# Kernel optimization log

Hardware: AMD Instinct MI355X
Metric: run time of the kernel (lower is better)

## Reference

```python
import jax, jax.numpy as jnp
import numpy as np

B, T, C = 2, 2048, 2048
N_HEAD, N_KV_HEAD = 16, 4
HEAD_DIM = C // N_HEAD  # 128
N_REP = N_HEAD // N_KV_HEAD  # 4


def setup_inputs() -> dict:
    key = jax.random.key(0)
    ks = jax.random.split(key, 5)
    x = jax.random.normal(ks[0], (B, T, C), dtype=jnp.float32)
    # RoPE freqs (theta=10000), real cos/sin form of torch's complex freqs_cis
    inv_freq = 1.0 / (10000.0 ** (jnp.arange(0, HEAD_DIM, 2, dtype=jnp.float32) / HEAD_DIM))
    angles = jnp.arange(T, dtype=jnp.float32)[:, None] * inv_freq[None, :]  # [T, HEAD_DIM//2]
    freqs_cos = jnp.cos(angles)
    freqs_sin = jnp.sin(angles)
    s = 0.02
    wq = jax.random.normal(ks[1], (C, C), dtype=jnp.float32) * s
    wk = jax.random.normal(ks[2], (N_KV_HEAD * HEAD_DIM, C), dtype=jnp.float32) * s
    wv = jax.random.normal(ks[3], (N_KV_HEAD * HEAD_DIM, C), dtype=jnp.float32) * s
    wo = jax.random.normal(ks[4], (C, C), dtype=jnp.float32) * s
    return {"x": x, "freqs_cos": freqs_cos, "freqs_sin": freqs_sin,
            "wq": wq, "wk": wk, "wv": wv, "wo": wo}


def _apply_rotary(t, cos, sin):
    # t: [B, T, H, D]; pairs (even, odd) treated as complex, multiplied by cos+i*sin
    tr = t.reshape(*t.shape[:-1], -1, 2)  # [B,T,H,D/2,2]
    t0, t1 = tr[..., 0], tr[..., 1]
    c = cos[None, :, None, :]  # [1,T,1,D/2]
    s = sin[None, :, None, :]
    out = jnp.stack([t0 * c - t1 * s, t0 * s + t1 * c], axis=-1)
    return out.reshape(t.shape)


def reference(x, freqs_cos, freqs_sin, wq, wk, wv, wo):
    b, t, _ = x.shape
    xq = (x @ wq.T).reshape(b, t, N_HEAD, HEAD_DIM)
    xk = (x @ wk.T).reshape(b, t, N_KV_HEAD, HEAD_DIM)
    xv = (x @ wv.T).reshape(b, t, N_KV_HEAD, HEAD_DIM)
    xq = _apply_rotary(xq, freqs_cos, freqs_sin)
    xk = _apply_rotary(xk, freqs_cos, freqs_sin)
    # GQA: repeat_interleave kv heads to n_head
    xk_r = jnp.repeat(xk, N_REP, axis=2)
    xv_r = jnp.repeat(xv, N_REP, axis=2)
    # [B,H,T,D]
    q = xq.transpose(0, 2, 1, 3)
    k = xk_r.transpose(0, 2, 1, 3)
    v = xv_r.transpose(0, 2, 1, 3)
    scale = 1.0 / jnp.sqrt(jnp.float32(HEAD_DIM))
    scores = jnp.einsum('bhtd,bhsd->bhts', q, k) * scale
    causal = jnp.tril(jnp.ones((t, t), dtype=bool))
    scores = jnp.where(causal[None, None], scores, jnp.finfo(scores.dtype).min)
    attn = jax.nn.softmax(scores, axis=-1)
    y = jnp.einsum('bhts,bhsd->bhtd', attn, v)
    y = y.transpose(0, 2, 1, 3).reshape(b, t, C)
    return y @ wo.T
```

## Files before the change

kernel.cpp:

```cpp
#include <hip/hip_runtime.h>

typedef __attribute__((ext_vector_type(8))) __bf16 bf16x8;
typedef __attribute__((ext_vector_type(4))) __bf16 bf16x4;
typedef __attribute__((ext_vector_type(4))) float floatx4;

#define MFMA16x16x32 __builtin_amdgcn_mfma_f32_16x16x32_bf16

__device__ __forceinline__ void async_load16(const void* g, void* l) {
  __builtin_amdgcn_global_load_lds((const __attribute__((address_space(1))) void*)g,
                                   (__attribute__((address_space(3))) void*)l, 16, 0, 0);
}

__global__ __launch_bounds__(256) void cast_all_kernel(const float* __restrict__ x,
                                                       const float* __restrict__ wq,
                                                       const float* __restrict__ wk,
                                                       const float* __restrict__ wv,
                                                       const float* __restrict__ wo,
                                                       __bf16* __restrict__ dst) {
  int i = blockIdx.x * blockDim.x + threadIdx.x;
  const float* src;
  int off;
  if (i < 2097152)      { src = x;  off = 0; }
  else if (i < 3145728) { src = wq; off = 2097152; }
  else if (i < 3407872) { src = wk; off = 3145728; }
  else if (i < 3670016) { src = wv; off = 3407872; }
  else                  { src = wo; off = 3670016; }
  float4 v = ((const float4*)src)[i - off];
  bf16x4 o;
  o[0] = (__bf16)v.x; o[1] = (__bf16)v.y; o[2] = (__bf16)v.z; o[3] = (__bf16)v.w;
  *(bf16x4*)(dst + (size_t)i * 4) = o;
}

template <int MODE, int BN>
__global__ __launch_bounds__(512, 1) void gemm_bt(const __bf16* __restrict__ A,
                                                  const __bf16* __restrict__ Bw,
                                                  float* __restrict__ C,
                                                  const float* __restrict__ cs,
                                                  const float* __restrict__ sn,
                                                  __bf16* __restrict__ qb,
                                                  __bf16* __restrict__ kb,
                                                  __bf16* __restrict__ vtg,
                                                  int M, int N, int K) {
  constexpr int NW = BN / 4;
  constexpr int NF = NW / 16;
  constexpr int NBI = BN / 64;
  __shared__ __bf16 As[2][256][64];
  __shared__ __bf16 Bs[2][BN][64];
  const int tid = threadIdx.x;
  const int wave = tid >> 6, lane = tid & 63;
  const int quad = lane >> 4, l16 = lane & 15;
  const int wm2 = wave >> 2, wn4 = wave & 3;
  const int lr = lane >> 3, ls = lane & 7;
  const int segg = ls ^ lr;

  const int nwg = gridDim.x;
  const int wg = (blockIdx.x & 7) * (nwg >> 3) + (blockIdx.x >> 3);
  const int GY = M >> 8;
  const int by = wg % GY, bx = wg / GY;
  const int row0 = by * 256, col0 = bx * BN;

  floatx4 acc[8][NF] = {};
  const __bf16* Ab = A + (size_t)row0 * K + segg * 8;
  const __bf16* Bb = Bw + (size_t)col0 * K + segg * 8;

  auto stage = [&](int sb, int k0) {
#pragma unroll
    for (int i = 0; i < 4; i++)
      async_load16(Ab + (size_t)(wave * 32 + i * 8 + lr) * K + k0,
                   &As[sb][wave * 32 + i * 8][0]);
#pragma unroll
    for (int j = 0; j < NBI; j++)
      async_load16(Bb + (size_t)(wave * (BN / 8) + j * 8 + lr) * K + k0,
                   &Bs[sb][wave * (BN / 8) + j * 8][0]);
  };

  const int NS = K >> 6;
  stage(0, 0);
  stage(1, 64);

#pragma unroll 2
  for (int s = 0; s < NS; s++) {
    const int c = s & 1;
    if (s == NS - 1) {
      asm volatile("s_waitcnt vmcnt(0)" ::: "memory");
    } else if constexpr (NBI == 3) {
      asm volatile("s_waitcnt vmcnt(7)" ::: "memory");
    } else {
      asm volatile("s_waitcnt vmcnt(6)" ::: "memory");
    }
    __builtin_amdgcn_s_barrier();

    bf16x8 af[2][8], bfr[2][NF];
#pragma unroll
    for (int kk = 0; kk < 2; kk++) {
#pragma unroll
      for (int mt = 0; mt < 8; mt++) {
        int row = wm2 * 128 + mt * 16 + l16;
        int seg = (kk * 4 + quad) ^ (row & 7);
        af[kk][mt] = *(const bf16x8*)&As[c][row][seg * 8];
      }
#pragma unroll
      for (int nt = 0; nt < NF; nt++) {
        int row = wn4 * NW + nt * 16 + l16;
        int seg = (kk * 4 + quad) ^ (row & 7);
        bfr[kk][nt] = *(const bf16x8*)&Bs[c][row][seg * 8];
      }
    }
    asm volatile("s_waitcnt lgkmcnt(0)" ::: "memory");
    __builtin_amdgcn_s_barrier();
    if (s + 2 < NS) stage(c, (s + 2) * 64);
    __builtin_amdgcn_s_setprio(1);
#pragma unroll
    for (int kk = 0; kk < 2; kk++)
#pragma unroll
      for (int mt = 0; mt < 8; mt++)
#pragma unroll
        for (int nt = 0; nt < NF; nt++)
          acc[mt][nt] = MFMA16x16x32(af[kk][mt], bfr[kk][nt], acc[mt][nt], 0, 0, 0);
    __builtin_amdgcn_s_setprio(0);
  }

  if (MODE == 0) {
#pragma unroll
    for (int mt = 0; mt < 8; mt++)
#pragma unroll
      for (int nt = 0; nt < NF; nt++)
#pragma unroll
        for (int r = 0; r < 4; r++) {
          int row = row0 + wm2 * 128 + mt * 16 + quad * 4 + r;
          int col = col0 + wn4 * NW + nt * 16 + l16;
          C[(size_t)row * N + col] = acc[mt][nt][r];
        }
  } else {
#pragma unroll
    for (int mt = 0; mt < 8; mt++)
#pragma unroll
      for (int nt = 0; nt < NF; nt++) {
        const int cbase = col0 + wn4 * NW + nt * 16;
        if (cbase < 2560) {
          const int c = cbase + l16;
#pragma unroll
          for (int r = 0; r < 4; r++) {
            int row = row0 + wm2 * 128 + mt * 16 + quad * 4 + r;
            int t = row & 2047;
            float v = acc[mt][nt][r];
            float vp = __shfl_xor(v, 1);
            int i = (c & 127) >> 1;
            float co = cs[t * 64 + i], si = sn[t * 64 + i];
            float rv = v * co + ((c & 1) ? vp : -vp) * si;
            if (cbase < 2048) {
              qb[(size_t)row * 2048 + c] = (__bf16)(rv * 0.1275411391f);
            } else {
              kb[(size_t)row * 512 + c - 2048] = (__bf16)rv;
            }
          }
        }
      }
    __bf16* Vl = &As[0][0][0] + wave * 2048;
    const int brow = row0 + wm2 * 128;
    const int bb = brow >> 11, trow = brow & 2047;
#pragma unroll
    for (int nt = 0; nt < NF; nt++) {
      const int cbase = col0 + wn4 * NW + nt * 16;
      if (cbase >= 2560) {
#pragma unroll
        for (int mt = 0; mt < 8; mt++)
#pragma unroll
          for (int r = 0; r < 4; r++)
            Vl[l16 * 128 + mt * 16 + quad * 4 + r] = (__bf16)acc[mt][nt][r];
        asm volatile("" ::: "memory");
        const int vB = cbase - 2560;
#pragma unroll
        for (int p = 0; p < 4; p++) {
          int vd = p * 4 + (lane >> 4);
          int t0 = (lane & 15) * 8;
          bf16x8 val = *(const bf16x8*)&Vl[vd * 128 + t0];
          *(bf16x8*)&vtg[((size_t)bb * 512 + vB + vd) * 2048 + trow + t0] = val;
        }
        asm volatile("" ::: "memory");
      }
    }
  }
}

__global__ __launch_bounds__(256, 2) void attn_kernel(const __bf16* __restrict__ qb,
                                                      const __bf16* __restrict__ kb,
                                                      const __bf16* __restrict__ vtg,
                                                      __bf16* __restrict__ yb) {
  const int id = blockIdx.x;
  const int kvh = id & 3, b = (id >> 2) & 1;
  const int pair = (id >> 3) & 1;
  const int tile = 63 - (id >> 4);
  const int tid = threadIdx.x, wave = tid >> 6, lane = tid & 63;
  const int ck = wave >> 1, hw = wave & 1;
  const int h = kvh * 4 + pair * 2 + hw;
  const int quad = lane >> 4, l16 = lane & 15;
  const int q0 = tile * 32;
  const int nkb = tile + 1;
  const int c0 = nkb >> 1;
  const int L1 = nkb - c0;

  __shared__ __bf16 Ks[2][64][128];
  __shared__ __bf16 Vt[2][128][64];
  __shared__ __bf16 Ps[4][2][16][32];

  const __bf16* kbase = kb + (size_t)b * 2048 * 512 + kvh * 128;
  const __bf16* vbase = vtg + ((size_t)b * 512 + kvh * 128) * 2048;

  const int klr4 = lane >> 4, kls = lane & 15;
  const __bf16* ksrc[4];
  char* kdst[4];
#pragma unroll
  for (int j = 0; j < 4; j++) {
    int lrow = hw * 16 + j * 4 + klr4;
    ksrc[j] = kbase + (size_t)lrow * 512 + (kls ^ (lrow & 7)) * 8;
    kdst[j] = (char*)Ks + (ck * 32 + hw * 16 + j * 4) * 256;
  }
  const int vdl = lane >> 2, vks = lane & 3;
  const __bf16* vsrc[4];
  char* vdst[4];
#pragma unroll
  for (int j = 0; j < 4; j++) {
    int d = hw * 64 + j * 16 + vdl;
    vsrc[j] = vbase + (size_t)d * 2048 + vks * 8;
    vdst[j] = (char*)Vt + d * 128 + (((ck * 4 + vks) ^ (d & 7)) * 16);
  }

  const int u16 = (quad ^ (l16 & 3)) * 16;
  const int b2_64 = (l16 & 4) ? 64 : 0;
  char* const kA0 = (char*)Ks + (ck * 32 + l16) * 256 + u16 + b2_64;
  char* const kB0 = kA0 + 64 - 2 * b2_64;
  char* const vrd0 = (char*)Vt + l16 * 128 + u16 + (((ck ^ (l16 >> 2)) & 1) ? 64 : 0);
  char* const psb = (char*)Ps + wave * 2048;
  char* const prd = psb + l16 * 64 + u16;
  const int h3 = (l16 >> 3) & 1;
  char* const pwE = psb + quad * 256 + (l16 & 7) * 2 + h3 * 16;
  char* const pwO = psb + quad * 256 + (l16 & 7) * 2 + 16 - h3 * 16;

  bf16x8 qf[2][4];
#pragma unroll
  for (int mt = 0; mt < 2; mt++)
#pragma unroll
    for (int kc = 0; kc < 4; kc++)
      qf[mt][kc] = *(const bf16x8*)(qb + (size_t)(b * 2048 + q0 + mt * 16 + l16) * 2048 +
                                    h * 128 + kc * 32 + quad * 8);
  bf16x8 ones;
#pragma unroll
  for (int j = 0; j < 8; j++) ones[j] = (__bf16)1.0f;
  floatx4 o[2][8] = {};
  floatx4 lsum[2] = {};

  {
    const int g0 = ck ? c0 : 0;
#pragma unroll
    for (int j = 0; j < 4; j++)
      async_load16(ksrc[j] + (size_t)g0 * 32 * 512, kdst[j]);
    bf16x8 vr[4];
#pragma unroll
    for (int j = 0; j < 4; j++) vr[j] = *(const bf16x8*)(vsrc[j] + g0 * 32);
#pragma unroll
    for (int j = 0; j < 4; j++) *(bf16x8*)(vdst[j]) = vr[j];
  }

  for (int it = 0; it < L1; it++) {
    const int cur = it & 1;
    const int bc = cur << 14, bn = (cur ^ 1) << 14;
    asm volatile("s_waitcnt lgkmcnt(0)" ::: "memory");
    asm volatile("s_barrier" ::: "memory");
    const bool pf = (it + 1 < L1);
    int gn = 0;
    if (pf) {
      gn = ck ? (c0 + it + 1) : min(it + 1, c0 > 0 ? c0 - 1 : 0);
#pragma unroll
      for (int j = 0; j < 4; j++)
        async_load16(ksrc[j] + (size_t)gn * 32 * 512, kdst[j] + bn);
      asm volatile("s_waitcnt vmcnt(4)" ::: "memory");
    } else {
      asm volatile("s_waitcnt vmcnt(0)" ::: "memory");
    }
    asm volatile("s_barrier" ::: "memory");

    floatx4 sacc[2][2] = {};
    __builtin_amdgcn_s_setprio(1);
#pragma unroll
    for (int kc = 0; kc < 4; kc++) {
      const char* kp = ((kc & 1) ? kB0 : kA0) + bc + (kc >> 1) * 128;
      bf16x8 bf0 = *(const bf16x8*)(kp);
      bf16x8 bf1 = *(const bf16x8*)(kp + 4096);
#pragma unroll
      for (int mt = 0; mt < 2; mt++) {
        sacc[mt][0] = MFMA16x16x32(qf[mt][kc], bf0, sacc[mt][0], 0, 0, 0);
        sacc[mt][1] = MFMA16x16x32(qf[mt][kc], bf1, sacc[mt][1], 0, 0, 0);
      }
    }
    __builtin_amdgcn_s_setprio(0);

    bf16x8 vr[4];
    if (pf) {
#pragma unroll
      for (int j = 0; j < 4; j++) vr[j] = *(const bf16x8*)(vsrc[j] + gn * 32);
    }

    const int gq = ck ? (c0 + it) : it;
    const bool diag = (ck == 1) && (it == L1 - 1);
    const bool inval = (ck == 0) && (it >= c0);
#pragma unroll
    for (int mt = 0; mt < 2; mt++)
#pragma unroll
      for (int r = 0; r < 4; r++) {
        const int qg = q0 + mt * 16 + quad * 4 + r;
#pragma unroll
        for (int nt = 0; nt < 2; nt++) {
          float p = __builtin_exp2f(sacc[mt][nt][r]);
          if (diag) { int keyg = gq * 32 + nt * 16 + l16; p = (keyg <= qg) ? p : 0.f; }
          if (inval) p = 0.f;
          char* w = (r & 1) ? pwO : pwE;
          *(__bf16*)(w + mt * 1024 + r * 64 + ((nt ^ ((r >> 1) & 1)) & 1) * 32) =
              (__bf16)p;
        }
      }

    __builtin_amdgcn_s_setprio(1);
    bf16x8 pa[2];
#pragma unroll
    for (int mt = 0; mt < 2; mt++) {
      pa[mt] = *(const bf16x8*)(prd + mt * 1024);
      lsum[mt] = MFMA16x16x32(pa[mt], ones, lsum[mt], 0, 0, 0);
    }
#pragma unroll
    for (int dt = 0; dt < 8; dt++) {
      bf16x8 vf = *(const bf16x8*)(vrd0 + bc + dt * 2048);
      o[0][dt] = MFMA16x16x32(pa[0], vf, o[0][dt], 0, 0, 0);
      o[1][dt] = MFMA16x16x32(pa[1], vf, o[1][dt], 0, 0, 0);
    }
    __builtin_amdgcn_s_setprio(0);

    if (pf) {
#pragma unroll
      for (int j = 0; j < 4; j++) *(bf16x8*)(vdst[j] + bn) = vr[j];
    }
  }

  asm volatile("s_barrier" ::: "memory");
  {
    char* mo = (char*)Ks + hw * 16384;
    char* ml = (char*)Vt + hw * 2048;
    if (ck == 1) {
#pragma unroll
      for (int mt = 0; mt < 2; mt++) {
#pragma unroll
        for (int dt = 0; dt < 8; dt++)
          *(floatx4*)(mo + ((mt * 8 + dt) * 64 + lane) * 16) = o[mt][dt];
        *(floatx4*)(ml + (mt * 64 + lane) * 16) = lsum[mt];
      }
    }
    asm volatile("s_waitcnt lgkmcnt(0)" ::: "memory");
    asm volatile("s_barrier" ::: "memory");
    if (ck == 0) {
#pragma unroll
      for (int mt = 0; mt < 2; mt++) {
        lsum[mt] += *(const floatx4*)(ml + (mt * 64 + lane) * 16);
        float inv[4];
#pragma unroll
        for (int r = 0; r < 4; r++) inv[r] = 1.f / lsum[mt][r];
#pragma unroll
        for (int dt = 0; dt < 8; dt++) {
          floatx4 op = *(const floatx4*)(mo + ((mt * 8 + dt) * 64 + lane) * 16);
#pragma unroll
          for (int r = 0; r < 4; r++) {
            int qg = q0 + mt * 16 + quad * 4 + r;
            yb[(size_t)(b * 2048 + qg) * 2048 + h * 128 + dt * 16 + l16] =
                (__bf16)((o[mt][dt][r] + op[r]) * inv[r]);
          }
        }
      }
    }
  }
}

extern "C" void kernel_launch(void* const* d_in, const int* in_sizes, int n_in,
                              void* d_out, int out_size, void* d_ws, size_t ws_size,
                              hipStream_t stream) {
  const float* x  = (const float*)d_in[0];
  const float* fc = (const float*)d_in[1];
  const float* fs = (const float*)d_in[2];
  const float* wq = (const float*)d_in[3];
  const float* wk = (const float*)d_in[4];
  const float* wv = (const float*)d_in[5];
  const float* wo = (const float*)d_in[6];
  float* out = (float*)d_out;
  char* ws = (char*)d_ws;

  __bf16* xb   = (__bf16*)(ws);
  __bf16* wqkv = (__bf16*)(ws + 16777216);
  __bf16* wob  = (__bf16*)(ws + 29360128);
  __bf16* qbuf = (__bf16*)(ws + 37748736);
  __bf16* kbuf = (__bf16*)(ws + 54525952);
  __bf16* vtg  = (__bf16*)(ws + 58720256);
  __bf16* ybuf = (__bf16*)(ws + 62914560);

  cast_all_kernel<<<18432, 256, 0, stream>>>(x, wq, wk, wv, wo, xb);

  gemm_bt<1, 192><<<256, 512, 0, stream>>>(xb, wqkv, nullptr, fc, fs,
                                           qbuf, kbuf, vtg, 4096, 3072, 2048);

  attn_kernel<<<1024, 256, 0, stream>>>(qbuf, kbuf, vtg, ybuf);

  gemm_bt<0, 128><<<256, 512, 0, stream>>>(ybuf, wob, out, nullptr, nullptr,
                                           nullptr, nullptr, nullptr, 4096, 2048, 2048);
}
```

Baseline: 303.2 us.

## Restructure attention: one wave per head, direct global K/V fragment loads, no LDS staging

The attention kernel drops the split-KV scheme, where two wave pairs each handled half the key range and merged through shared memory. Each of the four waves now owns one of the four query heads sharing a KV head and walks the whole causal key range. K fragments are register double-buffered and V fragments are loaded straight from global memory, so the K/V LDS tiles, async loads and barriers are gone. The grid is halved, and tiles are ordered so long and short ones interleave for load balance. In exchange, each wave fetches K/V from global or L2 on its own, losing the shared LDS reuse, and there are fewer blocks in flight.

```diff
diff --git a/kernel.cpp b/kernel.cpp
--- a/kernel.cpp
+++ b/kernel.cpp
@@ -189,54 +189,29 @@
                                                       __bf16* __restrict__ yb) {
   const int id = blockIdx.x;
   const int kvh = id & 3, b = (id >> 2) & 1;
-  const int pair = (id >> 3) & 1;
-  const int tile = 63 - (id >> 4);
+  const int tt = id >> 3;
+  const int tile = (tt < 32) ? (63 - tt) : (tt - 32);
   const int tid = threadIdx.x, wave = tid >> 6, lane = tid & 63;
-  const int ck = wave >> 1, hw = wave & 1;
-  const int h = kvh * 4 + pair * 2 + hw;
+  const int h = kvh * 4 + wave;
   const int quad = lane >> 4, l16 = lane & 15;
   const int q0 = tile * 32;
   const int nkb = tile + 1;
-  const int c0 = nkb >> 1;
-  const int L1 = nkb - c0;
-
-  __shared__ __bf16 Ks[2][64][128];
-  __shared__ __bf16 Vt[2][128][64];
+
   __shared__ __bf16 Ps[4][2][16][32];
 
   const __bf16* kbase = kb + (size_t)b * 2048 * 512 + kvh * 128;
   const __bf16* vbase = vtg + ((size_t)b * 512 + kvh * 128) * 2048;
 
-  const int klr4 = lane >> 4, kls = lane & 15;
-  const __bf16* ksrc[4];
-  char* kdst[4];
-#pragma unroll
-  for (int j = 0; j < 4; j++) {
-    int lrow = hw * 16 + j * 4 + klr4;
-    ksrc[j] = kbase + (size_t)lrow * 512 + (kls ^ (lrow & 7)) * 8;
-    kdst[j] = (char*)Ks + (ck * 32 + hw * 16 + j * 4) * 256;
-  }
-  const int vdl = lane >> 2, vks = lane & 3;
-  const __bf16* vsrc[4];
-  char* vdst[4];
-#pragma unroll
-  for (int j = 0; j < 4; j++) {
-    int d = hw * 64 + j * 16 + vdl;
-    vsrc[j] = vbase + (size_t)d * 2048 + vks * 8;
-    vdst[j] = (char*)Vt + d * 128 + (((ck * 4 + vks) ^ (d & 7)) * 16);
-  }
-
   const int u16 = (quad ^ (l16 & 3)) * 16;
-  const int b2_64 = (l16 & 4) ? 64 : 0;
-  char* const kA0 = (char*)Ks + (ck * 32 + l16) * 256 + u16 + b2_64;
-  char* const kB0 = kA0 + 64 - 2 * b2_64;
-  char* const vrd0 = (char*)Vt + l16 * 128 + u16 + (((ck ^ (l16 >> 2)) & 1) ? 64 : 0);
   char* const psb = (char*)Ps + wave * 2048;
   char* const prd = psb + l16 * 64 + u16;
   const int h3 = (l16 >> 3) & 1;
   char* const pwE = psb + quad * 256 + (l16 & 7) * 2 + h3 * 16;
   char* const pwO = psb + quad * 256 + (l16 & 7) * 2 + 16 - h3 * 16;
 
+  const __bf16* const kln = kbase + (size_t)l16 * 512 + quad * 8;
+  const __bf16* const vln = vbase + (size_t)l16 * 2048 + quad * 8;
+
   bf16x8 qf[2][4];
 #pragma unroll
   for (int mt = 0; mt < 2; mt++)
@@ -250,60 +225,37 @@
   floatx4 o[2][8] = {};
   floatx4 lsum[2] = {};
 
-  {
-    const int g0 = ck ? c0 : 0;
-#pragma unroll
-    for (int j = 0; j < 4; j++)
-      async_load16(ksrc[j] + (size_t)g0 * 32 * 512, kdst[j]);
-    bf16x8 vr[4];
-#pragma unroll
-    for (int j = 0; j < 4; j++) vr[j] = *(const bf16x8*)(vsrc[j] + g0 * 32);
-#pragma unroll
-    for (int j = 0; j < 4; j++) *(bf16x8*)(vdst[j]) = vr[j];
-  }
-
-  for (int it = 0; it < L1; it++) {
-    const int cur = it & 1;
-    const int bc = cur << 14, bn = (cur ^ 1) << 14;
-    asm volatile("s_waitcnt lgkmcnt(0)" ::: "memory");
-    asm volatile("s_barrier" ::: "memory");
-    const bool pf = (it + 1 < L1);
-    int gn = 0;
-    if (pf) {
-      gn = ck ? (c0 + it + 1) : min(it + 1, c0 > 0 ? c0 - 1 : 0);
-#pragma unroll
-      for (int j = 0; j < 4; j++)
-        async_load16(ksrc[j] + (size_t)gn * 32 * 512, kdst[j] + bn);
-      asm volatile("s_waitcnt vmcnt(4)" ::: "memory");
-    } else {
-      asm volatile("s_waitcnt vmcnt(0)" ::: "memory");
-    }
-    asm volatile("s_barrier" ::: "memory");
-
+  bf16x8 kfA[2][4], kfB[2][4];
+#pragma unroll
+  for (int nt = 0; nt < 2; nt++)
+#pragma unroll
+    for (int kc = 0; kc < 4; kc++)
+      kfA[nt][kc] = *(const bf16x8*)(kln + (size_t)(nt * 16) * 512 + kc * 32);
+
+  auto body = [&](bf16x8 (&kfC)[2][4], bf16x8 (&kfN)[2][4], int it) {
+    const int s0 = it * 32;
+    const bool last = (it == nkb - 1);
+    bf16x8 vf[8];
+#pragma unroll
+    for (int dt = 0; dt < 8; dt++)
+      vf[dt] = *(const bf16x8*)(vln + (size_t)(dt * 16) * 2048 + s0);
+    if (!last) {
+#pragma unroll
+      for (int nt = 0; nt < 2; nt++)
+#pragma unroll
+        for (int kc = 0; kc < 4; kc++)
+          kfN[nt][kc] = *(const bf16x8*)(kln + (size_t)(s0 + 32 + nt * 16) * 512 + kc * 32);
+    }
     floatx4 sacc[2][2] = {};
     __builtin_amdgcn_s_setprio(1);
 #pragma unroll
-    for (int kc = 0; kc < 4; kc++) {
-      const char* kp = ((kc & 1) ? kB0 : kA0) + bc + (kc >> 1) * 128;
-      bf16x8 bf0 = *(const bf16x8*)(kp);
-      bf16x8 bf1 = *(const bf16x8*)(kp + 4096);
+    for (int kc = 0; kc < 4; kc++)
 #pragma unroll
       for (int mt = 0; mt < 2; mt++) {
-        sacc[mt][0] = MFMA16x16x32(qf[mt][kc], bf0, sacc[mt][0], 0, 0, 0);
-        sacc[mt][1] = MFMA16x16x32(qf[mt][kc], bf1, sacc[mt][1], 0, 0, 0);
-      }
-    }
+        sacc[mt][0] = MFMA16x16x32(qf[mt][kc], kfC[0][kc], sacc[mt][0], 0, 0, 0);
+        sacc[mt][1] = MFMA16x16x32(qf[mt][kc], kfC[1][kc], sacc[mt][1], 0, 0, 0);
+      }
     __builtin_amdgcn_s_setprio(0);
-
-    bf16x8 vr[4];
-    if (pf) {
-#pragma unroll
-      for (int j = 0; j < 4; j++) vr[j] = *(const bf16x8*)(vsrc[j] + gn * 32);
-    }
-
-    const int gq = ck ? (c0 + it) : it;
-    const bool diag = (ck == 1) && (it == L1 - 1);
-    const bool inval = (ck == 0) && (it >= c0);
 #pragma unroll
     for (int mt = 0; mt < 2; mt++)
 #pragma unroll
@@ -312,14 +264,12 @@
 #pragma unroll
         for (int nt = 0; nt < 2; nt++) {
           float p = __builtin_exp2f(sacc[mt][nt][r]);
-          if (diag) { int keyg = gq * 32 + nt * 16 + l16; p = (keyg <= qg) ? p : 0.f; }
-          if (inval) p = 0.f;
+          if (last) { int keyg = s0 + nt * 16 + l16; p = (keyg <= qg) ? p : 0.f; }
           char* w = (r & 1) ? pwO : pwE;
           *(__bf16*)(w + mt * 1024 + r * 64 + ((nt ^ ((r >> 1) & 1)) & 1) * 32) =
               (__bf16)p;
         }
       }
-
     __builtin_amdgcn_s_setprio(1);
     bf16x8 pa[2];
 #pragma unroll
@@ -329,52 +279,33 @@
     }
 #pragma unroll
     for (int dt = 0; dt < 8; dt++) {
-      bf16x8 vf = *(const bf16x8*)(vrd0 + bc + dt * 2048);
-      o[0][dt] = MFMA16x16x32(pa[0], vf, o[0][dt], 0, 0, 0);
-      o[1][dt] = MFMA16x16x32(pa[1], vf, o[1][dt], 0, 0, 0);
+      o[0][dt] = MFMA16x16x32(pa[0], vf[dt], o[0][dt], 0, 0, 0);
+      o[1][dt] = MFMA16x16x32(pa[1], vf[dt], o[1][dt], 0, 0, 0);
     }
     __builtin_amdgcn_s_setprio(0);
-
-    if (pf) {
-#pragma unroll
-      for (int j = 0; j < 4; j++) *(bf16x8*)(vdst[j] + bn) = vr[j];
-    }
+  };
+
+  int it = 0;
+  for (;;) {
+    body(kfA, kfB, it);
+    if (++it >= nkb) break;
+    body(kfB, kfA, it);
+    if (++it >= nkb) break;
   }
 
-  asm volatile("s_barrier" ::: "memory");
-  {
-    char* mo = (char*)Ks + hw * 16384;
-    char* ml = (char*)Vt + hw * 2048;
-    if (ck == 1) {
-#pragma unroll
-      for (int mt = 0; mt < 2; mt++) {
-#pragma unroll
-        for (int dt = 0; dt < 8; dt++)
-          *(floatx4*)(mo + ((mt * 8 + dt) * 64 + lane) * 16) = o[mt][dt];
-        *(floatx4*)(ml + (mt * 64 + lane) * 16) = lsum[mt];
-      }
-    }
-    asm volatile("s_waitcnt lgkmcnt(0)" ::: "memory");
-    asm volatile("s_barrier" ::: "memory");
-    if (ck == 0) {
-#pragma unroll
-      for (int mt = 0; mt < 2; mt++) {
-        lsum[mt] += *(const floatx4*)(ml + (mt * 64 + lane) * 16);
-        float inv[4];
-#pragma unroll
-        for (int r = 0; r < 4; r++) inv[r] = 1.f / lsum[mt][r];
-#pragma unroll
-        for (int dt = 0; dt < 8; dt++) {
-          floatx4 op = *(const floatx4*)(mo + ((mt * 8 + dt) * 64 + lane) * 16);
-#pragma unroll
-          for (int r = 0; r < 4; r++) {
-            int qg = q0 + mt * 16 + quad * 4 + r;
-            yb[(size_t)(b * 2048 + qg) * 2048 + h * 128 + dt * 16 + l16] =
-                (__bf16)((o[mt][dt][r] + op[r]) * inv[r]);
-          }
-        }
-      }
-    }
+#pragma unroll
+  for (int mt = 0; mt < 2; mt++) {
+    float inv[4];
+#pragma unroll
+    for (int r = 0; r < 4; r++) inv[r] = 1.f / lsum[mt][r];
+#pragma unroll
+    for (int dt = 0; dt < 8; dt++)
+#pragma unroll
+      for (int r = 0; r < 4; r++) {
+        int qg = q0 + mt * 16 + quad * 4 + r;
+        yb[(size_t)(b * 2048 + qg) * 2048 + h * 128 + dt * 16 + l16] =
+            (__bf16)(o[mt][dt][r] * inv[r]);
+      }
   }
 }
 
@@ -404,7 +335,7 @@
   gemm_bt<1, 192><<<256, 512, 0, stream>>>(xb, wqkv, nullptr, fc, fs,
                                            qbuf, kbuf, vtg, 4096, 3072, 2048);
 
-  attn_kernel<<<1024, 256, 0, stream>>>(qbuf, kbuf, vtg, ybuf);
+  attn_kernel<<<512, 256, 0, stream>>>(qbuf, kbuf, vtg, ybuf);
 
   gemm_bt<0, 128><<<256, 512, 0, stream>>>(ybuf, wob, out, nullptr, nullptr,
                                            nullptr, nullptr, nullptr, 4096, 2048, 2048);
```

New measurement: 389.9 us. +28.6%, slower.
